# Optimization experiments

Measured on AMD Instinct MI355X. Metric: run time of the kernel, lower is better.

## Reference

```python
import jax, jax.numpy as jnp
import numpy as np

N_WIRES = 10
N_BLOCKS = 4
DIM = 2 ** N_WIRES


def _tables(n):
    # Basis-state bit tables. Wire 0 is the most-significant bit (torchquantum convention).
    s = np.arange(2 ** n)
    bits = (s[None, :] >> (n - 1 - np.arange(n))[:, None]) & 1  # [n, 2^n]
    zval = (1 - 2 * bits).astype(np.float32)  # PauliZ eigenvalue per wire per basis state
    # Composition of the circular CNOT ring (0,1),(1,2),...,(n-2,n-1),(n-1,0)
    # as a single basis permutation: state'[s] = state[P[s]].
    pairs = [(i, i + 1) for i in range(n - 1)] + [(n - 1, 0)]
    P = s.copy()
    for c, t in pairs:
        bit = (s >> (n - 1 - c)) & 1
        g = s ^ (bit << (n - 1 - t))  # CNOT maps new[s] = old[g(s)]
        P = P[g]
    return zval, P


_ZVAL_NP, _PERM_NP = _tables(N_WIRES)


def setup_inputs() -> dict:
    key = jax.random.key(0)
    k1, k2 = jax.random.split(key)
    x = jax.random.normal(k1, (2048, N_WIRES), jnp.float32)
    params = jax.random.normal(k2, (N_BLOCKS, 6, N_WIRES), jnp.float32)
    return {"x": x, "params": params}


def _rz_all(state, theta, zval):
    # RZ(theta_w) on every wire fused into one diagonal phase over the full statevector.
    # RZ = diag(e^{-i t/2}, e^{+i t/2}); exponent sign = -zval (bit0 -> -1).
    phase = jnp.exp((-0.5j) * (theta @ zval).astype(jnp.complex64))  # [2^n]
    return state * phase[None, :]


def _ry_all(state, theta, bsz):
    # RY(theta_w) on each wire w: 2x2 rotation applied along that wire's axis.
    for w in range(N_WIRES):
        left = 2 ** w
        right = DIM // (2 * left)
        s4 = state.reshape(bsz, left, 2, right)
        c = jnp.cos(theta[w] * 0.5)
        s_ = jnp.sin(theta[w] * 0.5)
        U = jnp.stack([jnp.stack([c, -s_]), jnp.stack([s_, c])]).astype(jnp.complex64)
        s4 = jnp.einsum('bixk,jx->bijk', s4, U)
        state = s4.reshape(bsz, DIM)
    return state


def reference(x, params):
    zval = jnp.asarray(_ZVAL_NP)
    perm = jnp.asarray(_PERM_NP)
    bsz = x.shape[0]
    state = jnp.zeros((bsz, DIM), jnp.complex64).at[:, 0].set(1.0)  # |0...0>
    for k in range(N_BLOCKS):
        p = params[k]
        # NOTE: the original module's "rx" layers are constructed with tq.RZ,
        # so each block is RZ, RY, RZ, CNOT-ring, RZ, RY, RZ, CNOT-ring.
        state = _rz_all(state, p[0], zval)
        state = _ry_all(state, p[1], bsz)
        state = _rz_all(state, p[2], zval)
        state = state[:, perm]
        state = _rz_all(state, p[3], zval)
        state = _ry_all(state, p[4], bsz)
        state = _rz_all(state, p[5], zval)
        state = state[:, perm]
        if k != N_BLOCKS - 1:
            # data re-uploading encoder: RZ(x[:, w]) on wire w, batch-dependent diagonal
            enc = jnp.exp((-0.5j) * (x @ zval).astype(jnp.complex64))  # [B, 2^n]
            state = state * enc
    probs = state.real ** 2 + state.imag ** 2  # [B, 2^n]
    out = probs @ zval.T  # MeasureAll PauliZ -> [B, n_wires]
    return out[None]  # [1, B, n_wires]
```

## Files before the change

kernel.cpp:

```cpp
#include <hip/hip_runtime.h>

#define NW 10

template<int CTRL>
__device__ __forceinline__ float fdpp(float v) {
    return __int_as_float(__builtin_amdgcn_mov_dpp(__float_as_int(v), CTRL, 0xF, 0xF, true));
}
template<int PAT>
__device__ __forceinline__ float fswz(float v) {
    return __int_as_float(__builtin_amdgcn_ds_swizzle(__float_as_int(v), PAT));
}

__global__ void precompute_kernel(const float* __restrict__ params, float2* __restrict__ tab) {
    const int d = blockIdx.x;
    const int j = threadIdx.x;
    if (d < 14) {
        int k, row;
        if (d < 3)       { k = d + 1;  row = 0; }
        else if (d < 7)  { k = d - 3;  row = 2; }
        else if (d < 11) { k = d - 7;  row = 3; }
        else             { k = d - 11; row = 5; }
        const float* th = params + (k * 6 + row) * NW;
        const int s = (((j >> 6) & 1) << 9) | ((j & 63) << 3) | (j >> 7);
        float ang = 0.f;
#pragma unroll
        for (int w = 0; w < NW; ++w)
            ang += th[w] * (((s >> (9 - w)) & 1) ? 0.5f : -0.5f);
        float sn, cs;
        __sincosf(ang, &sn, &cs);
        tab[d * 1024 + j] = make_float2(cs, sn);
    } else if (j < 80) {
        const int ry = j / NW, w = j % NW;
        const int k = ry >> 1, i = ry & 1;
        const float* th = params + (k * 6 + (i ? 4 : 1)) * NW;
        float sn, cs;
        __sincosf(0.5f * th[w], &sn, &cs);
        tab[14 * 1024 + j] = make_float2(cs, sn);
    }
}

__global__ __launch_bounds__(128, 4) void qsim_kernel(const float* __restrict__ x,
                                                      const float2* __restrict__ tab,
                                                      float* __restrict__ out) {
    __shared__ float2 buf[2][1024];
    __shared__ float sred[2][NW];

    const int t     = threadIdx.x;
    const int W     = t >> 6;
    const int lane  = t & 63;
    const int b     = blockIdx.x;
    const int ebase = lane | (W << 6);
    const float2* ry_tab = tab + 14 * 1024;

    float re[8], im[8];
#pragma unroll
    for (int r = 0; r < 8; ++r) { re[r] = 0.f; im[r] = 0.f; }
    if (t == 0) re[0] = 1.f;

    int geidx[8];
#pragma unroll
    for (int r = 0; r < 8; ++r) {
        const int s = (W << 9) | (lane << 3) | r;
        const int q = s ^ (s >> 1) ^ ((r & 1) * 0x300);
        geidx[r] = ((q >> 3) & 63) | (((q >> 9) & 1) << 6) | ((q & 7) << 7);
    }

    const float* xb = x + b * NW;
    float xr[8], xi[8];
    {
        float xv[NW];
#pragma unroll
        for (int w = 0; w < NW; ++w) xv[w] = xb[w];
        float A = 0.f;
#pragma unroll
        for (int w = 0; w < NW; ++w) A += xv[w];
        float hi = -0.5f * A + (W ? xv[0] : 0.f);
#pragma unroll
        for (int j = 0; j < 6; ++j)
            hi += ((lane >> j) & 1) ? xv[6 - j] : 0.f;
        float lo[8];
        lo[0] = 0.f;             lo[1] = xv[9];
        lo[2] = xv[8];           lo[3] = xv[8] + xv[9];
        lo[4] = xv[7];           lo[5] = xv[7] + xv[9];
        lo[6] = xv[7] + xv[8];   lo[7] = xv[7] + xv[8] + xv[9];
#pragma unroll
        for (int r = 0; r < 8; ++r)
            __sincosf(hi + lo[r], &xi[r], &xr[r]);
    }

    int bs = 0;

    auto tdiag = [&](int d) {
        const float2* tb = tab + (d << 10) + ebase;
#pragma unroll
        for (int r = 0; r < 8; ++r) {
            const float2 p = tb[r << 7];
            const float a = re[r], bb = im[r];
            re[r] = a * p.x - bb * p.y;
            im[r] = a * p.y + bb * p.x;
        }
    };
    auto txdiag = [&](int d) {
        const float2* tb = tab + (d << 10) + ebase;
#pragma unroll
        for (int r = 0; r < 8; ++r) {
            const float2 p = tb[r << 7];
            const float cx = p.x * xr[r] - p.y * xi[r];
            const float sx = p.x * xi[r] + p.y * xr[r];
            const float a = re[r], bb = im[r];
            re[r] = a * cx - bb * sx;
            im[r] = a * sx + bb * cx;
        }
    };

    auto ry = [&](int ridx) {
        const float2* rt = ry_tab + ridx * NW;
#pragma unroll
        for (int kb = 0; kb < 3; ++kb) {
            const float2 cw = rt[9 - kb];
            const int m = 1 << kb;
#pragma unroll
            for (int r = 0; r < 8; ++r) {
                if (!(r & m)) {
                    const int r2 = r | m;
                    float a = re[r], bb = re[r2];
                    re[r]  = cw.x * a - cw.y * bb;
                    re[r2] = cw.y * a + cw.x * bb;
                    float ai = im[r], bi = im[r2];
                    im[r]  = cw.x * ai - cw.y * bi;
                    im[r2] = cw.y * ai + cw.x * bi;
                }
            }
        }
        {
            const float2 cw = rt[6];
            const float ss = (lane & 1) ? cw.y : -cw.y;
#pragma unroll
            for (int r = 0; r < 8; ++r) {
                float pre = fdpp<0xB1>(re[r]);
                float pim = fdpp<0xB1>(im[r]);
                re[r] = cw.x * re[r] + ss * pre;
                im[r] = cw.x * im[r] + ss * pim;
            }
        }
        {
            const float2 cw = rt[5];
            const float ss = (lane & 2) ? cw.y : -cw.y;
#pragma unroll
            for (int r = 0; r < 8; ++r) {
                float pre = fdpp<0x4E>(re[r]);
                float pim = fdpp<0x4E>(im[r]);
                re[r] = cw.x * re[r] + ss * pre;
                im[r] = cw.x * im[r] + ss * pim;
            }
        }
        {
            const float2 cw = rt[4];
            const float ss = (lane & 4) ? cw.y : -cw.y;
#pragma unroll
            for (int r = 0; r < 8; ++r) {
                float pre = fswz<0x101F>(re[r]);
                float pim = fswz<0x101F>(im[r]);
                re[r] = cw.x * re[r] + ss * pre;
                im[r] = cw.x * im[r] + ss * pim;
            }
        }
        {
            const float2 cw = rt[3];
            const float ss = (lane & 8) ? cw.y : -cw.y;
#pragma unroll
            for (int r = 0; r < 8; ++r) {
                float pre = fdpp<0x128>(re[r]);
                float pim = fdpp<0x128>(im[r]);
                re[r] = cw.x * re[r] + ss * pre;
                im[r] = cw.x * im[r] + ss * pim;
            }
        }
        {
            const float2 cw = rt[2];
            const float ss = (lane & 16) ? cw.y : -cw.y;
#pragma unroll
            for (int r = 0; r < 8; ++r) {
                float pre = fswz<0x401F>(re[r]);
                float pim = fswz<0x401F>(im[r]);
                re[r] = cw.x * re[r] + ss * pre;
                im[r] = cw.x * im[r] + ss * pim;
            }
        }
        {
            const float2 cw = rt[1];
            const float ss = (lane & 32) ? cw.y : -cw.y;
#pragma unroll
            for (int r = 0; r < 8; ++r) {
                float pre = __shfl_xor(re[r], 32, 64);
                float pim = __shfl_xor(im[r], 32, 64);
                re[r] = cw.x * re[r] + ss * pre;
                im[r] = cw.x * im[r] + ss * pim;
            }
        }
        {
            const float2 cw = rt[0];
            float2* B = buf[bs]; bs ^= 1;
#pragma unroll
            for (int r = 0; r < 8; ++r)
                B[ebase + (r << 7)] = make_float2(re[r], im[r]);
            __syncthreads();
            const float ss = W ? cw.y : -cw.y;
            const int pb = ebase ^ 64;
#pragma unroll
            for (int r = 0; r < 8; ++r) {
                const float2 p = B[pb + (r << 7)];
                re[r] = cw.x * re[r] + ss * p.x;
                im[r] = cw.x * im[r] + ss * p.y;
            }
        }
    };

    auto perm = [&]() {
        float2* B = buf[bs]; bs ^= 1;
#pragma unroll
        for (int r = 0; r < 8; ++r)
            B[ebase + (r << 7)] = make_float2(re[r], im[r]);
        __syncthreads();
#pragma unroll
        for (int r = 0; r < 8; ++r) {
            const float2 p = B[geidx[r]];
            re[r] = p.x;
            im[r] = p.y;
        }
    };

#pragma unroll 1
    for (int k = 0; k < 4; ++k) {
        if (k > 0) txdiag(k - 1);
        ry(2 * k);
        tdiag(3 + k);
        perm();
        tdiag(7 + k);
        ry(2 * k + 1);
        if (k < 3) tdiag(11 + k);
        perm();
    }

    float pr[8];
#pragma unroll
    for (int r = 0; r < 8; ++r) pr[r] = re[r] * re[r] + im[r] * im[r];
    float S = 0.f;
#pragma unroll
    for (int r = 0; r < 8; ++r) S += pr[r];

    float acc[NW];
    acc[0] = W ? -S : S;
#pragma unroll
    for (int w = 1; w <= 6; ++w) {
        const int j = 6 - w;
        acc[w] = ((lane >> j) & 1) ? -S : S;
    }
#pragma unroll
    for (int w = 7; w < NW; ++w) {
        const int kb = 9 - w;
        float tt = 0.f;
#pragma unroll
        for (int r = 0; r < 8; ++r)
            tt += ((r >> kb) & 1) ? -pr[r] : pr[r];
        acc[w] = tt;
    }
#pragma unroll
    for (int w = 0; w < NW; ++w) {
        float a = acc[w];
        a += fdpp<0xB1>(a);
        a += fdpp<0x4E>(a);
        a += fswz<0x101F>(a);
        a += fdpp<0x128>(a);
        a += fswz<0x401F>(a);
        a += __shfl_xor(a, 32, 64);
        acc[w] = a;
    }
    if (lane == 0) {
#pragma unroll
        for (int w = 0; w < NW; ++w) sred[W][w] = acc[w];
    }
    __syncthreads();
    if (t < NW) out[b * NW + t] = sred[0][t] + sred[1][t];
}

extern "C" void kernel_launch(void* const* d_in, const int* in_sizes, int n_in,
                              void* d_out, int out_size, void* d_ws, size_t ws_size,
                              hipStream_t stream) {
    const float* x      = (const float*)d_in[0];
    const float* params = (const float*)d_in[1];
    float* out          = (float*)d_out;
    float2* tab         = (float2*)d_ws;
    (void)in_sizes; (void)n_in; (void)out_size; (void)ws_size;
    precompute_kernel<<<15, 1024, 0, stream>>>(params, tab);
    qsim_kernel<<<2048, 128, 0, stream>>>(x, tab, out);
}
```

Measured before the change: 86.31 us.

## Split each statevector across four waves with four amplitudes per thread

Remaps the 1024-amplitude statevector from 2 waves × 8 amplitudes per lane to 4 waves × 4 amplitudes per lane. Two wires now live on the wave index: their RY rotations are combined into a single 4-way shared-memory exchange, and the diagonal tables and permutation indices are re-laid out to match. The aim is to cut per-thread register use and serial work and raise occupancy. In exchange, each block has more threads meeting at barriers and more shared-memory reads per RY step.

Result: slower. 89.19 us (+3.3%).

```diff
diff --git a/kernel.cpp b/kernel.cpp
--- a/kernel.cpp
+++ b/kernel.cpp
@@ -21,7 +21,8 @@
         else if (d < 11) { k = d - 7;  row = 3; }
         else             { k = d - 11; row = 5; }
         const float* th = params + (k * 6 + row) * NW;
-        const int s = (((j >> 6) & 1) << 9) | ((j & 63) << 3) | (j >> 7);
+        const int lane = j & 63, r = (j >> 6) & 3, W = (j >> 8) & 3;
+        const int s = (W << 8) | (lane << 2) | r;
         float ang = 0.f;
 #pragma unroll
         for (int w = 0; w < NW; ++w)
@@ -39,34 +40,34 @@
     }
 }
 
-__global__ __launch_bounds__(128, 4) void qsim_kernel(const float* __restrict__ x,
+__global__ __launch_bounds__(256, 8) void qsim_kernel(const float* __restrict__ x,
                                                       const float2* __restrict__ tab,
                                                       float* __restrict__ out) {
     __shared__ float2 buf[2][1024];
-    __shared__ float sred[2][NW];
+    __shared__ float sred[4][NW];
 
     const int t     = threadIdx.x;
     const int W     = t >> 6;
     const int lane  = t & 63;
     const int b     = blockIdx.x;
-    const int ebase = lane | (W << 6);
+    const int ebase = lane | (W << 8);
     const float2* ry_tab = tab + 14 * 1024;
 
-    float re[8], im[8];
-#pragma unroll
-    for (int r = 0; r < 8; ++r) { re[r] = 0.f; im[r] = 0.f; }
+    float re[4], im[4];
+#pragma unroll
+    for (int r = 0; r < 4; ++r) { re[r] = 0.f; im[r] = 0.f; }
     if (t == 0) re[0] = 1.f;
 
-    int geidx[8];
-#pragma unroll
-    for (int r = 0; r < 8; ++r) {
-        const int s = (W << 9) | (lane << 3) | r;
+    int geidx[4];
+#pragma unroll
+    for (int r = 0; r < 4; ++r) {
+        const int s = (W << 8) | (lane << 2) | r;
         const int q = s ^ (s >> 1) ^ ((r & 1) * 0x300);
-        geidx[r] = ((q >> 3) & 63) | (((q >> 9) & 1) << 6) | ((q & 7) << 7);
+        geidx[r] = ((q >> 2) & 63) | ((q & 3) << 6) | ((q >> 8) << 8);
     }
 
     const float* xb = x + b * NW;
-    float xr[8], xi[8];
+    float xr[4], xi[4];
     {
         float xv[NW];
 #pragma unroll
@@ -74,17 +75,17 @@
         float A = 0.f;
 #pragma unroll
         for (int w = 0; w < NW; ++w) A += xv[w];
-        float hi = -0.5f * A + (W ? xv[0] : 0.f);
+        float hi = -0.5f * A;
+        if (W & 2) hi += xv[0];
+        if (W & 1) hi += xv[1];
 #pragma unroll
         for (int j = 0; j < 6; ++j)
-            hi += ((lane >> j) & 1) ? xv[6 - j] : 0.f;
-        float lo[8];
-        lo[0] = 0.f;             lo[1] = xv[9];
-        lo[2] = xv[8];           lo[3] = xv[8] + xv[9];
-        lo[4] = xv[7];           lo[5] = xv[7] + xv[9];
-        lo[6] = xv[7] + xv[8];   lo[7] = xv[7] + xv[8] + xv[9];
-#pragma unroll
-        for (int r = 0; r < 8; ++r)
+            hi += ((lane >> j) & 1) ? xv[7 - j] : 0.f;
+        float lo[4];
+        lo[0] = 0.f;     lo[1] = xv[9];
+        lo[2] = xv[8];   lo[3] = xv[8] + xv[9];
+#pragma unroll
+        for (int r = 0; r < 4; ++r)
             __sincosf(hi + lo[r], &xi[r], &xr[r]);
     }
 
@@ -93,8 +94,8 @@
     auto tdiag = [&](int d) {
         const float2* tb = tab + (d << 10) + ebase;
 #pragma unroll
-        for (int r = 0; r < 8; ++r) {
-            const float2 p = tb[r << 7];
+        for (int r = 0; r < 4; ++r) {
+            const float2 p = tb[r << 6];
             const float a = re[r], bb = im[r];
             re[r] = a * p.x - bb * p.y;
             im[r] = a * p.y + bb * p.x;
@@ -103,8 +104,8 @@
     auto txdiag = [&](int d) {
         const float2* tb = tab + (d << 10) + ebase;
 #pragma unroll
-        for (int r = 0; r < 8; ++r) {
-            const float2 p = tb[r << 7];
+        for (int r = 0; r < 4; ++r) {
+            const float2 p = tb[r << 6];
             const float cx = p.x * xr[r] - p.y * xi[r];
             const float sx = p.x * xi[r] + p.y * xr[r];
             const float a = re[r], bb = im[r];
@@ -116,11 +117,11 @@
     auto ry = [&](int ridx) {
         const float2* rt = ry_tab + ridx * NW;
 #pragma unroll
-        for (int kb = 0; kb < 3; ++kb) {
+        for (int kb = 0; kb < 2; ++kb) {
             const float2 cw = rt[9 - kb];
             const int m = 1 << kb;
 #pragma unroll
-            for (int r = 0; r < 8; ++r) {
+            for (int r = 0; r < 4; ++r) {
                 if (!(r & m)) {
                     const int r2 = r | m;
                     float a = re[r], bb = re[r2];
@@ -133,85 +134,88 @@
             }
         }
         {
+            const float2 cw = rt[7];
+            const float ss = (lane & 1) ? cw.y : -cw.y;
+#pragma unroll
+            for (int r = 0; r < 4; ++r) {
+                float pre = fdpp<0xB1>(re[r]), pim = fdpp<0xB1>(im[r]);
+                re[r] = cw.x * re[r] + ss * pre;
+                im[r] = cw.x * im[r] + ss * pim;
+            }
+        }
+        {
             const float2 cw = rt[6];
-            const float ss = (lane & 1) ? cw.y : -cw.y;
-#pragma unroll
-            for (int r = 0; r < 8; ++r) {
-                float pre = fdpp<0xB1>(re[r]);
-                float pim = fdpp<0xB1>(im[r]);
+            const float ss = (lane & 2) ? cw.y : -cw.y;
+#pragma unroll
+            for (int r = 0; r < 4; ++r) {
+                float pre = fdpp<0x4E>(re[r]), pim = fdpp<0x4E>(im[r]);
                 re[r] = cw.x * re[r] + ss * pre;
                 im[r] = cw.x * im[r] + ss * pim;
             }
         }
         {
             const float2 cw = rt[5];
-            const float ss = (lane & 2) ? cw.y : -cw.y;
-#pragma unroll
-            for (int r = 0; r < 8; ++r) {
-                float pre = fdpp<0x4E>(re[r]);
-                float pim = fdpp<0x4E>(im[r]);
+            const float ss = (lane & 4) ? cw.y : -cw.y;
+#pragma unroll
+            for (int r = 0; r < 4; ++r) {
+                float pre = fswz<0x101F>(re[r]), pim = fswz<0x101F>(im[r]);
                 re[r] = cw.x * re[r] + ss * pre;
                 im[r] = cw.x * im[r] + ss * pim;
             }
         }
         {
             const float2 cw = rt[4];
-            const float ss = (lane & 4) ? cw.y : -cw.y;
-#pragma unroll
-            for (int r = 0; r < 8; ++r) {
-                float pre = fswz<0x101F>(re[r]);
-                float pim = fswz<0x101F>(im[r]);
+            const float ss = (lane & 8) ? cw.y : -cw.y;
+#pragma unroll
+            for (int r = 0; r < 4; ++r) {
+                float pre = fdpp<0x128>(re[r]), pim = fdpp<0x128>(im[r]);
                 re[r] = cw.x * re[r] + ss * pre;
                 im[r] = cw.x * im[r] + ss * pim;
             }
         }
         {
             const float2 cw = rt[3];
-            const float ss = (lane & 8) ? cw.y : -cw.y;
-#pragma unroll
-            for (int r = 0; r < 8; ++r) {
-                float pre = fdpp<0x128>(re[r]);
-                float pim = fdpp<0x128>(im[r]);
+            const float ss = (lane & 16) ? cw.y : -cw.y;
+#pragma unroll
+            for (int r = 0; r < 4; ++r) {
+                float pre = fswz<0x401F>(re[r]), pim = fswz<0x401F>(im[r]);
                 re[r] = cw.x * re[r] + ss * pre;
                 im[r] = cw.x * im[r] + ss * pim;
             }
         }
         {
             const float2 cw = rt[2];
-            const float ss = (lane & 16) ? cw.y : -cw.y;
-#pragma unroll
-            for (int r = 0; r < 8; ++r) {
-                float pre = fswz<0x401F>(re[r]);
-                float pim = fswz<0x401F>(im[r]);
-                re[r] = cw.x * re[r] + ss * pre;
-                im[r] = cw.x * im[r] + ss * pim;
-            }
-        }
-        {
-            const float2 cw = rt[1];
             const float ss = (lane & 32) ? cw.y : -cw.y;
 #pragma unroll
-            for (int r = 0; r < 8; ++r) {
-                float pre = __shfl_xor(re[r], 32, 64);
-                float pim = __shfl_xor(im[r], 32, 64);
-                re[r] = cw.x * re[r] + ss * pre;
-                im[r] = cw.x * im[r] + ss * pim;
-            }
-        }
-        {
-            const float2 cw = rt[0];
+            for (int r = 0; r < 4; ++r) {
+                float pre = __shfl_xor(re[r], 32, 64), pim = __shfl_xor(im[r], 32, 64);
+                re[r] = cw.x * re[r] + ss * pre;
+                im[r] = cw.x * im[r] + ss * pim;
+            }
+        }
+        {
+            const float2 c0 = rt[0], c1 = rt[1];
             float2* B = buf[bs]; bs ^= 1;
 #pragma unroll
-            for (int r = 0; r < 8; ++r)
-                B[ebase + (r << 7)] = make_float2(re[r], im[r]);
+            for (int r = 0; r < 4; ++r)
+                B[ebase + (r << 6)] = make_float2(re[r], im[r]);
             __syncthreads();
-            const float ss = W ? cw.y : -cw.y;
-            const int pb = ebase ^ 64;
-#pragma unroll
-            for (int r = 0; r < 8; ++r) {
-                const float2 p = B[pb + (r << 7)];
-                re[r] = cw.x * re[r] + ss * p.x;
-                im[r] = cw.x * im[r] + ss * p.y;
+            const float a1 = (W & 2) ? c0.y : -c0.y;
+            const float b1 = (W & 1) ? c1.y : -c1.y;
+            const float k00 = c0.x * c1.x;
+            const float k01 = c0.x * b1;
+            const float k10 = a1 * c1.x;
+            const float k11 = a1 * b1;
+            const int p1 = ebase ^ (1 << 8);
+            const int p2 = ebase ^ (2 << 8);
+            const int p3 = ebase ^ (3 << 8);
+#pragma unroll
+            for (int r = 0; r < 4; ++r) {
+                const float2 q1 = B[p1 + (r << 6)];
+                const float2 q2 = B[p2 + (r << 6)];
+                const float2 q3 = B[p3 + (r << 6)];
+                re[r] = k00 * re[r] + k01 * q1.x + k10 * q2.x + k11 * q3.x;
+                im[r] = k00 * im[r] + k01 * q1.y + k10 * q2.y + k11 * q3.y;
             }
         }
     };
@@ -219,11 +223,11 @@
     auto perm = [&]() {
         float2* B = buf[bs]; bs ^= 1;
 #pragma unroll
-        for (int r = 0; r < 8; ++r)
-            B[ebase + (r << 7)] = make_float2(re[r], im[r]);
+        for (int r = 0; r < 4; ++r)
+            B[ebase + (r << 6)] = make_float2(re[r], im[r]);
         __syncthreads();
 #pragma unroll
-        for (int r = 0; r < 8; ++r) {
+        for (int r = 0; r < 4; ++r) {
             const float2 p = B[geidx[r]];
             re[r] = p.x;
             im[r] = p.y;
@@ -242,28 +246,29 @@
         perm();
     }
 
-    float pr[8];
-#pragma unroll
-    for (int r = 0; r < 8; ++r) pr[r] = re[r] * re[r] + im[r] * im[r];
+    float pr[4];
+#pragma unroll
+    for (int r = 0; r < 4; ++r) pr[r] = re[r] * re[r] + im[r] * im[r];
     float S = 0.f;
 #pragma unroll
-    for (int r = 0; r < 8; ++r) S += pr[r];
+    for (int r = 0; r < 4; ++r) S += pr[r];
 
     float acc[NW];
-    acc[0] = W ? -S : S;
-#pragma unroll
-    for (int w = 1; w <= 6; ++w) {
-        const int j = 6 - w;
+    acc[0] = (W & 2) ? -S : S;
+    acc[1] = (W & 1) ? -S : S;
+#pragma unroll
+    for (int w = 2; w <= 7; ++w) {
+        const int j = 7 - w;
         acc[w] = ((lane >> j) & 1) ? -S : S;
     }
-#pragma unroll
-    for (int w = 7; w < NW; ++w) {
-        const int kb = 9 - w;
-        float tt = 0.f;
-#pragma unroll
-        for (int r = 0; r < 8; ++r)
-            tt += ((r >> kb) & 1) ? -pr[r] : pr[r];
-        acc[w] = tt;
+    {
+        float t8 = 0.f, t9 = 0.f;
+#pragma unroll
+        for (int r = 0; r < 4; ++r) {
+            t8 += (r & 2) ? -pr[r] : pr[r];
+            t9 += (r & 1) ? -pr[r] : pr[r];
+        }
+        acc[8] = t8; acc[9] = t9;
     }
 #pragma unroll
     for (int w = 0; w < NW; ++w) {
@@ -281,7 +286,7 @@
         for (int w = 0; w < NW; ++w) sred[W][w] = acc[w];
     }
     __syncthreads();
-    if (t < NW) out[b * NW + t] = sred[0][t] + sred[1][t];
+    if (t < NW) out[b * NW + t] = sred[0][t] + sred[1][t] + sred[2][t] + sred[3][t];
 }
 
 extern "C" void kernel_launch(void* const* d_in, const int* in_sizes, int n_in,
@@ -293,5 +298,5 @@
     float2* tab         = (float2*)d_ws;
     (void)in_sizes; (void)n_in; (void)out_size; (void)ws_size;
     precompute_kernel<<<15, 1024, 0, stream>>>(params, tab);
-    qsim_kernel<<<2048, 128, 0, stream>>>(x, tab, out);
-}
+    qsim_kernel<<<2048, 256, 0, stream>>>(x, tab, out);
+}
```
